# Optimization experiments

Hardware: AMD Instinct MI355X
Metric: run time of the kernel (lower is better)

Reference implementation:

```python
import jax, jax.numpy as jnp
import numpy as np

# SOLO decoupled-head postprocessing config (TrainConfig)
GRIDS = (40, 36, 24, 16, 12)
STRIDES = (4.0, 8.0, 16.0, 32.0, 64.0)
NMS_PRE = 500
SCORE_THR = 0.1
MASK_THR = 0.005
UPDATE_THR = 0.001
SIGMA = 2.0
MAX_PER_IMG = 100
NUM_CLASSES = 80


def _cell_meta():
    """Per-flattened-cell metadata across the 5 FPN levels (static)."""
    trans_diff, seg_diff, num_grids, strides = [], [], [], []
    t, s = 0, 0
    for g, st in zip(GRIDS, STRIDES):
        n = g * g
        trans_diff.append(np.full(n, t, np.int32))
        seg_diff.append(np.full(n, s, np.int32))
        num_grids.append(np.full(n, g, np.int32))
        strides.append(np.full(n, st, np.float32))
        t += n
        s += g
    return (jnp.asarray(np.concatenate(trans_diff)),
            jnp.asarray(np.concatenate(seg_diff)),
            jnp.asarray(np.concatenate(num_grids)),
            jnp.asarray(np.concatenate(strides)))


def setup_inputs() -> dict:
    key = jax.random.key(0)
    k1, k2, k3 = jax.random.split(key, 3)
    n_cells = sum(g * g for g in GRIDS)   # 3872
    n_rows = sum(GRIDS)                   # 128
    H, W = 200, 304                        # stride-4 map of an 800x1216 image
    return {
        "cate_preds": jax.random.uniform(k1, (n_cells, NUM_CLASSES), jnp.float32),
        "seg_preds_x": jax.random.uniform(k2, (n_rows, H, W), jnp.float32),
        "seg_preds_y": jax.random.uniform(k3, (n_rows, H, W), jnp.float32),
        "ori_h": 427,
        "ori_w": 640,
    }


def _matrix_nms(hardf, labels, scores, sum_masks):
    """Matrix NMS with gaussian decay. hardf: [n, h, w] float, descending scores."""
    n = hardf.shape[0]
    flat = hardf.reshape(n, -1)                      # [n, h*w]
    inter = flat @ flat.T                            # [n, n] pairwise intersection
    union = sum_masks[None, :] + sum_masks[:, None] - inter
    iou = jnp.where(union > 0, inter / jnp.maximum(union, 1e-12), 0.0)
    tri = jnp.triu(jnp.ones((n, n), jnp.float32), 1)  # cols > rows (strict upper)
    same = (labels[None, :] == labels[:, None]) & (labels[:, None] >= 0)
    decay_iou = iou * tri * same.astype(jnp.float32)  # [n, n]
    comp = decay_iou.max(axis=0)                      # max IoU with higher-scored same-class
    decay_m = jnp.exp(-SIGMA * decay_iou ** 2)
    comp_m = jnp.exp(-SIGMA * comp[:, None] ** 2)     # compensate[i, j] = f(comp[i])
    coeff = (decay_m / comp_m).min(axis=0)            # [n]
    return scores * coeff


def reference(cate_preds, seg_preds_x, seg_preds_y, ori_h, ori_w):
    trans_diff, seg_diff, num_grids, strides = _cell_meta()
    C = cate_preds.shape[1]
    flat = cate_preds.reshape(-1)
    flat = jnp.where(flat > SCORE_THR, flat, -1.0)
    scores, idx = jax.lax.top_k(flat, NMS_PRE)        # fixed-size candidate set
    loc = idx // C
    labels = (idx % C).astype(jnp.int32)
    valid = scores > SCORE_THR

    td, sd = trans_diff[loc], seg_diff[loc]
    ng, st = num_grids[loc], strides[loc]
    y_inds = (loc - td) // ng + sd
    x_inds = (loc - td) % ng + sd

    soft = seg_preds_x[x_inds] * seg_preds_y[y_inds]  # [N, H, W]
    hard = soft > MASK_THR
    sum_masks = hard.sum(axis=(1, 2)).astype(jnp.float32)
    keep = valid & (sum_masks > st)
    seg_score = (soft * hard).sum(axis=(1, 2)) / jnp.maximum(sum_masks, 1e-6)
    scores = jnp.where(keep, scores * seg_score, 0.0)
    keepf = keep.astype(jnp.float32)
    hardf = hard.astype(jnp.float32) * keepf[:, None, None]
    sum_masks = sum_masks * keepf
    labels = jnp.where(keep, labels, -1)

    # descending sort (matrix NMS assumes descending scores)
    order = jnp.argsort(-scores)
    scores, labels = scores[order], labels[order]
    soft, hardf, sum_masks = soft[order], hardf[order], sum_masks[order]

    scores = _matrix_nms(hardf, labels, scores, sum_masks)
    scores = jnp.where(scores > UPDATE_THR, scores, 0.0)

    top_scores, top_idx = jax.lax.top_k(scores, MAX_PER_IMG)
    top_soft = soft[top_idx]                          # [100, H, W]
    top_labels = labels[top_idx]

    H, W = top_soft.shape[1], top_soft.shape[2]
    up = jax.image.resize(top_soft, (MAX_PER_IMG, H * 4, W * 4), method="bilinear")
    up = jax.image.resize(up, (MAX_PER_IMG, ori_h, ori_w), method="bilinear")
    seg_masks = (up > MASK_THR).astype(jnp.float32)
    return seg_masks, top_labels, top_scores
```

## Files before the change

### kernel.cpp

```cpp
#include <hip/hip_runtime.h>
#include <stdint.h>

typedef unsigned int u32;
typedef unsigned long long u64;

#define NCELLS  3872
#define NCLS    80
#define NFLAT   309760
#define NPRE    500
#define NPAD    512
#define HH      200
#define WW      304
#define NPIX    60800
#define NWORDS  950
#define MSTRIDE 960
#define MAXOUT  100
#define OH      427
#define OW      640
#define MH      800
#define MW      1216
#define MAXG    4096
#define MAXPAIRS 16384
#define OUT_LBL 27328000
#define OUT_SCR 27328100
#define ROWS_PER_BLK 2
#define NRBLK 214

#define S_THR 0.1f
#define M_THR 0.005f
#define U_THR 0.001f

#define OFF_HIST1   0u
#define OFF_META    263168u
#define ZERO_BYTES  262144u
#define OFF_CAND    263424u
#define OFF_RAW     296192u
#define OFF_LOC     298240u
#define OFF_LABEL   300288u
#define OFF_XIND    302336u
#define OFF_YIND    304384u
#define OFF_STRIDE  306432u
#define OFF_SMF     308480u
#define OFF_SCORE   310528u
#define OFF_LABELK  312576u
#define OFF_ORDER   314624u
#define OFF_SSCORE  316672u
#define OFF_TOPC    318720u
#define OFF_PAIRI   319232u
#define OFF_PAIRIOU 384768u
#define OFF_W1YT0   450304u
#define OFF_W1YA    453504u
#define OFF_W1YB    456704u
#define OFF_W1XT0   459904u
#define OFF_W1XA    464768u
#define OFF_W1XB    469632u
#define OFF_W2YS    474496u
#define OFF_W2YW    476224u
#define OFF_W2XS    483072u
#define OFF_W2XW    485632u
#define OFF_MASKS   495872u
#define OFF_MASKT   4335872u
#define OFF_PARTD   8227072u
#define WS_NEED     12118272u

#define P_U32(off) ((u32*)(ws + (off)))
#define P_I32(off) ((int*)(ws + (off)))
#define P_F32(off) ((float*)(ws + (off)))
#define P_U64(off) ((u64*)(ws + (off)))

__device__ __forceinline__ void levelMeta(int loc, int& td, int& sd, int& ng, float& st) {
  if (loc < 1600)      { td = 0;    sd = 0;   ng = 40; st = 4.f;  }
  else if (loc < 2896) { td = 1600; sd = 40;  ng = 36; st = 8.f;  }
  else if (loc < 3472) { td = 2896; sd = 76;  ng = 24; st = 16.f; }
  else if (loc < 3728) { td = 3472; sd = 100; ng = 16; st = 32.f; }
  else                 { td = 3728; sd = 116; ng = 12; st = 64.f; }
}

__device__ __forceinline__ u32 vbin(float v) {
  int b = (int)(v * 65536.0f);
  if (b > 65535) b = 65535;
  if (b < 0) b = 0;
  return (u32)b;
}

__device__ __forceinline__ u64 shflx64(u64 v, int m) {
  u32 lo = (u32)v, hi = (u32)(v >> 32);
  lo = (u32)__shfl_xor((int)lo, m);
  hi = (u32)__shfl_xor((int)hi, m);
  return (((u64)hi) << 32) | lo;
}

__global__ void kh1(const float* __restrict__ cate, char* __restrict__ ws) {
  int i = blockIdx.x * 256 + threadIdx.x;
  if (i >= NFLAT / 4) return;
  float4 v = ((const float4*)cate)[i];
  u32* h = P_U32(OFF_HIST1);
  if (v.x > S_THR) atomicAdd(&h[vbin(v.x)], 1u);
  if (v.y > S_THR) atomicAdd(&h[vbin(v.y)], 1u);
  if (v.z > S_THR) atomicAdd(&h[vbin(v.z)], 1u);
  if (v.w > S_THR) atomicAdd(&h[vbin(v.w)], 1u);
}

__global__ __launch_bounds__(1024) void kselw(const float* __restrict__ cate, char* __restrict__ ws) {
  __shared__ u64 sk[MAXG];
  __shared__ u32 cs[1024];
  __shared__ u32 sfx[1024];
  __shared__ int cbS;
  __shared__ u32 aboveS;
  __shared__ u32 gcnt;
  __shared__ u32 cutS;
  int tid = threadIdx.x;
  const u32* h = P_U32(OFF_HIST1);
  u32 s = 0;
  for (int b = 0; b < 64; b++) s += h[tid * 64 + b];
  sfx[tid] = s;
  if (tid == 0) { cbS = -1; gcnt = 0; cutS = 0; }
  __syncthreads();
  for (int off = 1; off < 1024; off <<= 1) {
    u32 v = (tid + off < 1024) ? sfx[tid + off] : 0u;
    __syncthreads();
    sfx[tid] += v;
    __syncthreads();
  }
  u32 nxt = (tid < 1023) ? sfx[tid + 1] : 0u;
  if (sfx[tid] >= NPRE && nxt < NPRE) { cbS = tid; aboveS = nxt; }
  __syncthreads();
  if (cbS >= 0) {
    int cb = cbS;
    if (tid < 64) cs[tid] = h[cb * 64 + tid];
    __syncthreads();
    if (tid == 0) {
      u32 cum = aboveS;
      u32 bin = (u32)(cb * 64);
      for (int b = 63; b >= 0; b--) {
        u32 hb = cs[b];
        if (cum + hb >= NPRE) { bin = (u32)(cb * 64 + b); break; }
        cum += hb;
      }
      cutS = bin;
    }
  }
  __syncthreads();
  u32 cutbin = cutS;
  const float4* cate4 = (const float4*)cate;
  for (int i = tid; i < NFLAT / 4; i += 1024) {
    float4 v = cate4[i];
    #pragma unroll
    for (int q = 0; q < 4; q++) {
      float f = (q == 0) ? v.x : (q == 1) ? v.y : (q == 2) ? v.z : v.w;
      if (f > S_THR && vbin(f) >= cutbin) {
        u32 pos = atomicAdd(&gcnt, 1u);
        if (pos < MAXG) sk[pos] = (((u64)__float_as_uint(f)) << 32) | (u32)(~(u32)(i * 4 + q));
      }
    }
  }
  __syncthreads();
  int G = (int)gcnt; if (G > MAXG) G = MAXG;
  int n = NPAD;
  while (n < G) n <<= 1;
  for (int i = G + tid; i < n; i += 1024) sk[i] = 0ull;
  __syncthreads();
  if (n == NPAD) {
    u64 key = (tid < NPAD) ? sk[tid] : 0ull;
    __syncthreads();
    for (int k = 2; k <= NPAD; k <<= 1) {
      for (int j = k >> 1; j > 0; j >>= 1) {
        bool up = ((tid & k) == 0);
        u64 other;
        if (j < 64) {
          other = shflx64(key, j);
        } else {
          if (tid < NPAD) sk[tid] = key;
          __syncthreads();
          other = sk[(tid ^ j) & (NPAD - 1)];
          __syncthreads();
        }
        bool takeMax = (((tid & j) == 0) == up);
        u64 nk = takeMax ? (key > other ? key : other) : (key < other ? key : other);
        if (tid < NPAD) key = nk;
      }
    }
    if (tid < NPAD) sk[tid] = key;
    __syncthreads();
  } else {
    for (int k = 2; k <= n; k <<= 1) {
      for (int j = k >> 1; j > 0; j >>= 1) {
        for (int i = tid; i < n; i += 1024) {
          int l = i ^ j;
          if (l > i) {
            u64 a = sk[i], b = sk[l];
            bool sw = ((i & k) == 0) ? (a < b) : (a > b);
            if (sw) { sk[i] = b; sk[l] = a; }
          }
        }
        __syncthreads();
      }
    }
  }
  if (tid < NPAD) {
    float rawv = -1.f; int lab = -1, xi = 0, yi = 0; float st = 3.0e38f;
    if (tid < NPRE && tid < G) {
      u64 key = sk[tid];
      u32 b = (u32)(key >> 32);
      u32 idx = ~((u32)(key & 0xffffffffu));
      rawv = __uint_as_float(b);
      int loc = (int)(idx / (u32)NCLS);
      lab = (int)(idx - (u32)loc * NCLS);
      int td, sd, ng; levelMeta(loc, td, sd, ng, st);
      int rel = loc - td;
      int row = rel / ng;
      yi = row + sd;
      xi = (rel - row * ng) + sd;
    }
    P_F32(OFF_RAW)[tid] = rawv;
    P_I32(OFF_LABEL)[tid] = lab;
    P_I32(OFF_XIND)[tid] = xi;
    P_I32(OFF_YIND)[tid] = yi;
    P_F32(OFF_STRIDE)[tid] = st;
    P_F32(OFF_SCORE)[tid] = 0.f;
    P_I32(OFF_LABELK)[tid] = -1;
    P_F32(OFF_SMF)[tid] = 0.f;
  }
  int t = tid;
  for (int r = t; r < MH; r += 1024) {
    float s1 = ((float)r + 0.5f) * 0.25f - 0.5f;
    int t0 = (int)floorf(s1);
    float f = s1 - (float)t0;
    float wa = 1.f - f, wb = f;
    bool ia = (t0 >= 0) && (t0 < HH);
    bool ib = ((t0 + 1) >= 0) && ((t0 + 1) < HH);
    float tw = (ia ? wa : 0.f) + (ib ? wb : 0.f);
    float na = ia ? (wa / tw) : 0.f;
    float nb = ib ? (wb / tw) : 0.f;
    int base; float A, B;
    if (t0 < 0) { base = 0; A = nb; B = 0.f; }
    else if (t0 >= HH - 1) { base = HH - 2; A = 0.f; B = na; }
    else { base = t0; A = na; B = nb; }
    P_I32(OFF_W1YT0)[r] = base;
    P_F32(OFF_W1YA)[r] = A;
    P_F32(OFF_W1YB)[r] = B;
  }
  for (int c = t; c < MW; c += 1024) {
    float s1 = ((float)c + 0.5f) * 0.25f - 0.5f;
    int t0 = (int)floorf(s1);
    float f = s1 - (float)t0;
    float wa = 1.f - f, wb = f;
    bool ia = (t0 >= 0) && (t0 < WW);
    bool ib = ((t0 + 1) >= 0) && ((t0 + 1) < WW);
    float tw = (ia ? wa : 0.f) + (ib ? wb : 0.f);
    float na = ia ? (wa / tw) : 0.f;
    float nb = ib ? (wb / tw) : 0.f;
    int base; float A, B;
    if (t0 < 0) { base = 0; A = nb; B = 0.f; }
    else if (t0 >= WW - 1) { base = WW - 2; A = 0.f; B = na; }
    else { base = t0; A = na; B = nb; }
    P_I32(OFF_W1XT0)[c] = base;
    P_F32(OFF_W1XA)[c] = A;
    P_F32(OFF_W1XB)[c] = B;
  }
  for (int o = t; o < OH; o += 1024) {
    const float inv = (float)(800.0 / 427.0);
    float s2 = ((float)o + 0.5f) * inv - 0.5f;
    int rA = (int)ceilf(s2 - inv);
    int rB = (int)floorf(s2 + inv);
    if (rA < 0) rA = 0;
    if (rB > MH - 1) rB = MH - 1;
    float tot = 0.f;
    for (int r = rA; r <= rB; r++) {
      float x = fabsf(s2 - (float)r) / inv;
      float w = 1.f - x; if (w < 0.f) w = 0.f;
      tot += w;
    }
    int base = rA; if (base > MH - 4) base = MH - 4;
    float o4[4] = {0.f, 0.f, 0.f, 0.f};
    for (int r = rA; r <= rB; r++) {
      float x = fabsf(s2 - (float)r) / inv;
      float w = 1.f - x; if (w < 0.f) w = 0.f;
      o4[r - base] += w / tot;
    }
    P_I32(OFF_W2YS)[o] = base;
    float* wp = P_F32(OFF_W2YW) + o * 4;
    wp[0] = o4[0]; wp[1] = o4[1]; wp[2] = o4[2]; wp[3] = o4[3];
  }
  for (int o = t; o < OW; o += 1024) {
    const float inv = (float)(1216.0 / 640.0);
    float s2 = ((float)o + 0.5f) * inv - 0.5f;
    int rA = (int)ceilf(s2 - inv);
    int rB = (int)floorf(s2 + inv);
    if (rA < 0) rA = 0;
    if (rB > MW - 1) rB = MW - 1;
    float tot = 0.f;
    for (int r = rA; r <= rB; r++) {
      float x = fabsf(s2 - (float)r) / inv;
      float w = 1.f - x; if (w < 0.f) w = 0.f;
      tot += w;
    }
    int base = rA; if (base > MW - 4) base = MW - 4;
    float o4[4] = {0.f, 0.f, 0.f, 0.f};
    for (int r = rA; r <= rB; r++) {
      float x = fabsf(s2 - (float)r) / inv;
      float w = 1.f - x; if (w < 0.f) w = 0.f;
      o4[r - base] += w / tot;
    }
    P_I32(OFF_W2XS)[o] = base;
    float* wp = P_F32(OFF_W2XW) + o * 4;
    wp[0] = o4[0]; wp[1] = o4[1]; wp[2] = o4[2]; wp[3] = o4[3];
  }
}

__global__ __launch_bounds__(256) void kmaskA(const float* __restrict__ segx, const float* __restrict__ segy,
                                              char* __restrict__ ws) {
  __shared__ float lx[128 * 64];
  __shared__ float ly[128 * 64];
  int w0 = blockIdx.x;
  int base = w0 << 6;
  int tid = threadIdx.x;
  for (int idx = tid; idx < 128 * 64; idx += 256) {
    int r = idx >> 6, col = idx & 63;
    int sw = col ^ (r & 63);
    lx[(r << 6) + sw] = segx[(size_t)r * NPIX + base + col];
    ly[(r << 6) + sw] = segy[(size_t)r * NPIX + base + col];
  }
  __syncthreads();
  const int* xind = P_I32(OFF_XIND);
  const int* yind = P_I32(OFF_YIND);
  u64* maskT = P_U64(OFF_MASKT) + (size_t)w0 * NPAD;
  double* partD = (double*)(ws + OFF_PARTD) + (size_t)w0 * NPAD;
  for (int c = tid; c < NPRE; c += 256) {
    int xi = xind[c], yi = yind[c];
    const float* rx = &lx[xi << 6];
    const float* ry = &ly[yi << 6];
    int xk = xi & 63, yk = yi & 63;
    u32 lo = 0, hi = 0;
    double sum = 0.0;
    #pragma unroll 8
    for (int p = 0; p < 32; p++) {
      float s = rx[p ^ xk] * ry[p ^ yk];
      if (s > M_THR) { lo |= (1u << p); sum += (double)s; }
    }
    #pragma unroll 8
    for (int p = 32; p < 64; p++) {
      float s = rx[p ^ xk] * ry[p ^ yk];
      if (s > M_THR) { hi |= (1u << (p - 32)); sum += (double)s; }
    }
    maskT[c] = (((u64)hi) << 32) | lo;
    partD[c] = sum;
  }
}

__global__ __launch_bounds__(256) void kmaskBT(char* __restrict__ ws) {
  __shared__ u64 tile[64][65];
  int b = blockIdx.x;
  int tid = threadIdx.x;
  if (b < NPRE) {
    __shared__ double cd[256];
    __shared__ int ci[256];
    int c = b;
    const u64* maskT = P_U64(OFF_MASKT);
    const double* partD = (const double*)(ws + OFF_PARTD);
    double ds = 0.0; int cnt = 0;
    for (int w = tid; w < NWORDS; w += 256) {
      ds += partD[(size_t)w * NPAD + c];
      cnt += (int)__popcll(maskT[(size_t)w * NPAD + c]);
    }
    cd[tid] = ds; ci[tid] = cnt;
    __syncthreads();
    for (int s2 = 128; s2 > 0; s2 >>= 1) {
      if (tid < s2) { ci[tid] += ci[tid + s2]; cd[tid] += cd[tid + s2]; }
      __syncthreads();
    }
    if (tid == 0) {
      float sm = (float)ci[0];
      float rawv = P_F32(OFF_RAW)[c];
      bool valid = rawv > S_THR;
      bool keep = valid && (sm > P_F32(OFF_STRIDE)[c]);
      float ssf = (float)cd[0];
      float segsc = ssf / fmaxf(sm, 1e-6f);
      P_F32(OFF_SCORE)[c] = keep ? (rawv * segsc) : 0.f;
      P_F32(OFF_SMF)[c] = keep ? sm : 0.f;
      P_I32(OFF_LABELK)[c] = keep ? P_I32(OFF_LABEL)[c] : -1;
    }
  } else {
    int q = b - NPRE;
    int w0 = (q % 15) << 6;
    int c0 = (q / 15) << 6;
    const u64* maskT = P_U64(OFF_MASKT);
    for (int idx = tid; idx < 64 * 64; idx += 256) {
      int rw = idx >> 6, cc = idx & 63;
      int w = w0 + rw;
      tile[rw][cc] = (w < NWORDS) ? maskT[(size_t)w * NPAD + (c0 + cc)] : 0ull;
    }
    __syncthreads();
    u64* masks = P_U64(OFF_MASKS);
    for (int idx = tid; idx < 64 * 64; idx += 256) {
      int rc = idx >> 6, wwi = idx & 63;
      int c = c0 + rc, w = w0 + wwi;
      if (c < NPRE && w < NWORDS) masks[(size_t)c * MSTRIDE + w] = tile[wwi][rc];
    }
  }
}

__global__ __launch_bounds__(256) void kmask(const float* __restrict__ segx, const float* __restrict__ segy,
                                             char* __restrict__ ws) {
  int c = blockIdx.x;
  int tid = threadIdx.x;
  int lane = tid & 63, wv = tid >> 6;
  const float* X = segx + (size_t)P_I32(OFF_XIND)[c] * NPIX;
  const float* Y = segy + (size_t)P_I32(OFF_YIND)[c] * NPIX;
  u64* mrow = P_U64(OFF_MASKS) + (size_t)c * MSTRIDE;
  int cnt = 0;
  double ssum = 0.0;
  for (int w0 = wv; w0 < NWORDS; w0 += 4) {
    int p = (w0 << 6) + lane;
    float s = X[p] * Y[p];
    bool b = s > M_THR;
    u64 bal = __ballot(b ? 1 : 0);
    if (lane == 0) mrow[w0] = bal;
    if (b) { cnt++; ssum += (double)s; }
  }
  __shared__ int ci[256];
  __shared__ double cd[256];
  ci[tid] = cnt; cd[tid] = ssum;
  __syncthreads();
  for (int s2 = 128; s2 > 0; s2 >>= 1) {
    if (tid < s2) { ci[tid] += ci[tid + s2]; cd[tid] += cd[tid + s2]; }
    __syncthreads();
  }
  if (tid == 0) {
    float sm = (float)ci[0];
    float rawv = P_F32(OFF_RAW)[c];
    bool valid = rawv > S_THR;
    bool keep = valid && (sm > P_F32(OFF_STRIDE)[c]);
    float ssf = (float)cd[0];
    float segsc = ssf / fmaxf(sm, 1e-6f);
    P_F32(OFF_SCORE)[c] = keep ? (rawv * segsc) : 0.f;
    P_F32(OFF_SMF)[c] = keep ? sm : 0.f;
    P_I32(OFF_LABELK)[c] = keep ? P_I32(OFF_LABEL)[c] : -1;
  }
}

__global__ __launch_bounds__(512) void ksp(char* __restrict__ ws) {
  __shared__ u64 sk[NPAD];
  __shared__ short slab[NPAD];
  __shared__ u32 scan[NPAD];
  int t = threadIdx.x;
  float sc = (t < NPRE) ? P_F32(OFF_SCORE)[t] : 0.f;
  u64 key = (((u64)__float_as_uint(sc)) << 32) | (u32)(NPAD - 1 - t);
  for (int k = 2; k <= NPAD; k <<= 1) {
    for (int j = k >> 1; j > 0; j >>= 1) {
      bool up = ((t & k) == 0);
      u64 other;
      if (j < 64) {
        other = shflx64(key, j);
      } else {
        sk[t] = key;
        __syncthreads();
        other = sk[t ^ j];
        __syncthreads();
      }
      bool takeMax = (((t & j) == 0) == up);
      key = takeMax ? (key > other ? key : other) : (key < other ? key : other);
    }
  }
  int ord = NPAD - 1 - (int)(key & 0xffffffffu);
  P_I32(OFF_ORDER)[t] = ord;
  P_F32(OFF_SSCORE)[t] = __uint_as_float((u32)(key >> 32));
  const int* labelK = P_I32(OFF_LABELK);
  int lab = (t < NPRE) ? labelK[ord] : -1;
  slab[t] = (short)lab;
  __syncthreads();
  u32 cnt = 0;
  if (lab >= 0) {
    short lj = (short)lab;
    for (int i = 0; i < t; i++) if (slab[i] == lj) cnt++;
  }
  scan[t] = cnt;
  __syncthreads();
  for (int off = 1; off < NPAD; off <<= 1) {
    u32 v = (t >= off) ? scan[t - off] : 0u;
    __syncthreads();
    scan[t] += v;
    __syncthreads();
  }
  if (t == NPAD - 1) {
    u32 tot = scan[t];
    P_U32(OFF_META)[4] = (tot > MAXPAIRS) ? MAXPAIRS : tot;
  }
  if (lab >= 0 && cnt) {
    u32 pos = scan[t] - cnt;
    short lj = (short)lab;
    u32* pairI = P_U32(OFF_PAIRI);
    for (int i = 0; i < t; i++) {
      if (slab[i] == lj) {
        if (pos < MAXPAIRS) pairI[pos] = (((u32)i) << 16) | (u32)t;
        pos++;
      }
    }
  }
}

__global__ __launch_bounds__(64) void kpiou(char* __restrict__ ws) {
  int P = (int)P_U32(OFF_META)[4]; if (P > MAXPAIRS) P = MAXPAIRS;
  const int* order = P_I32(OFF_ORDER);
  const float* smf = P_F32(OFF_SMF);
  const u64* masks = P_U64(OFF_MASKS);
  for (int p = blockIdx.x; p < P; p += gridDim.x) {
    u32 ij = P_U32(OFF_PAIRI)[p];
    int oi = order[ij >> 16];
    int oj = order[ij & 0xffffu];
    const u64* mi = masks + (size_t)oi * MSTRIDE;
    const u64* mj = masks + (size_t)oj * MSTRIDE;
    int inter = 0;
    for (int w = threadIdx.x; w < NWORDS; w += 64)
      inter += (int)__popcll(mi[w] & mj[w]);
    for (int off = 32; off > 0; off >>= 1)
      inter += __shfl_down(inter, off);
    if (threadIdx.x == 0) {
      float fi = (float)inter;
      float uni = (smf[oj] + smf[oi]) - fi;
      float iou = (uni > 0.f) ? (fi / fmaxf(uni, 1e-12f)) : 0.f;
      P_F32(OFF_PAIRIOU)[p] = iou;
    }
  }
}

__global__ __launch_bounds__(512) void knms(char* __restrict__ ws, float* __restrict__ out) {
  __shared__ int compI[NPAD];
  __shared__ int coefI[NPAD];
  __shared__ u64 sk[NPAD];
  int t = threadIdx.x;
  int P = (int)P_U32(OFF_META)[4]; if (P > MAXPAIRS) P = MAXPAIRS;
  const u32* pairI = P_U32(OFF_PAIRI);
  const float* pairIou = P_F32(OFF_PAIRIOU);
  const float* sscore = P_F32(OFF_SSCORE);
  const int* order = P_I32(OFF_ORDER);
  const int* labelK = P_I32(OFF_LABELK);
  int* topc = P_I32(OFF_TOPC);
  compI[t] = 0;
  coefI[t] = __float_as_int(1.0f);
  __syncthreads();
  for (int p = t; p < P; p += 512) {
    int j = (int)(pairI[p] & 0xffffu);
    atomicMax(&compI[j], __float_as_int(pairIou[p]));
  }
  __syncthreads();
  for (int p = t; p < P; p += 512) {
    u32 ij = pairI[p];
    int i = (int)(ij >> 16), j = (int)(ij & 0xffffu);
    float x = pairIou[p];
    float c = __int_as_float(compI[i]);
    float x2 = x * x, c2 = c * c;
    float r = (float)exp(-2.0 * ((double)x2 - (double)c2));
    atomicMin(&coefI[j], __float_as_int(r));
  }
  __syncthreads();
  float ns = 0.f;
  if (t < NPRE) {
    ns = sscore[t] * __int_as_float(coefI[t]);
    ns = (ns > U_THR) ? ns : 0.f;
  }
  u64 key = (((u64)__float_as_uint(ns)) << 32) | (u32)(NPAD - 1 - t);
  for (int k = 2; k <= NPAD; k <<= 1) {
    for (int j = k >> 1; j > 0; j >>= 1) {
      bool up = ((t & k) == 0);
      u64 other;
      if (j < 64) {
        other = shflx64(key, j);
      } else {
        sk[t] = key;
        __syncthreads();
        other = sk[t ^ j];
        __syncthreads();
      }
      bool takeMax = (((t & j) == 0) == up);
      key = takeMax ? (key > other ? key : other) : (key < other ? key : other);
    }
  }
  if (t < MAXOUT) {
    int pos = NPAD - 1 - (int)(key & 0xffffffffu);
    int cand = order[pos];
    topc[t] = cand;
    out[OUT_LBL + t] = (float)labelK[cand];
    out[OUT_SCR + t] = __uint_as_float((u32)(key >> 32));
  }
}

__global__ __launch_bounds__(256) void kout(const float* __restrict__ segx, const float* __restrict__ segy,
                                            char* __restrict__ ws, float* __restrict__ out) {
  __shared__ float t1s[6][WW];
  __shared__ float yrs[2][MW];
  int flat = blockIdx.x;
  int w = (flat & 7) * 2675 + (flat >> 3);
  int kk = w / NRBLK;
  int r2 = w - kk * NRBLK;
  int oy0 = r2 * ROWS_PER_BLK;
  int nrow = (oy0 + 1 < OH) ? 2 : 1;
  int tid = threadIdx.x;
  int cand = P_I32(OFF_TOPC)[kk];
  const float* X = segx + (size_t)P_I32(OFF_XIND)[cand] * NPIX;
  const float* Y = segy + (size_t)P_I32(OFF_YIND)[cand] * NPIX;
  const int* w2ys = P_I32(OFF_W2YS);
  int rb = w2ys[oy0];
  const int* w1yT0 = P_I32(OFF_W1YT0);
  const float* w1yA = P_F32(OFF_W1YA);
  const float* w1yB = P_F32(OFF_W1YB);
  int smin = w1yT0[rb];
  float Ay[6], By[6]; int i0a[6];
  #pragma unroll
  for (int mr = 0; mr < 6; mr++) {
    int r = rb + mr; if (r > MH - 1) r = MH - 1;
    i0a[mr] = w1yT0[r] - smin;
    Ay[mr] = w1yA[r];
    By[mr] = w1yB[r];
  }
  {
    int r0 = smin;     if (r0 > HH - 1) r0 = HH - 1;
    int r1 = smin + 1; if (r1 > HH - 1) r1 = HH - 1;
    int r2s = smin + 2; if (r2s > HH - 1) r2s = HH - 1;
    int r3 = smin + 3; if (r3 > HH - 1) r3 = HH - 1;
    const float* X0 = X + r0 * WW; const float* Y0 = Y + r0 * WW;
    const float* X1 = X + r1 * WW; const float* Y1 = Y + r1 * WW;
    const float* X2 = X + r2s * WW; const float* Y2 = Y + r2s * WW;
    const float* X3 = X + r3 * WW; const float* Y3 = Y + r3 * WW;
    for (int u = tid; u < WW; u += 256) {
      float s0 = X0[u] * Y0[u];
      float s1 = X1[u] * Y1[u];
      float s2 = X2[u] * Y2[u];
      float s3 = X3[u] * Y3[u];
      #pragma unroll
      for (int mr = 0; mr < 6; mr++) {
        int i0 = i0a[mr];
        float sa, sb;
        if (i0 == 0)      { sa = s0; sb = s1; }
        else if (i0 == 1) { sa = s1; sb = s2; }
        else              { sa = s2; sb = s3; }
        t1s[mr][u] = fmaf(By[mr], sb, Ay[mr] * sa);
      }
    }
  }
  __syncthreads();
  const int* w1xT0 = P_I32(OFF_W1XT0);
  const float* w1xA = P_F32(OFF_W1XA);
  const float* w1xB = P_F32(OFF_W1XB);
  float4 wy0 = *(const float4*)(P_F32(OFF_W2YW) + oy0 * 4);
  int oy1 = (nrow == 2) ? (oy0 + 1) : oy0;
  float4 wy1 = *(const float4*)(P_F32(OFF_W2YW) + oy1 * 4);
  int off1 = w2ys[oy1] - rb;
  for (int cc = tid; cc < MW; cc += 256) {
    int u0 = w1xT0[cc];
    float xa = w1xA[cc], xb = w1xB[cc];
    float up0 = fmaf(xb, t1s[0][u0 + 1], xa * t1s[0][u0]);
    float up1 = fmaf(xb, t1s[1][u0 + 1], xa * t1s[1][u0]);
    float up2 = fmaf(xb, t1s[2][u0 + 1], xa * t1s[2][u0]);
    float up3 = fmaf(xb, t1s[3][u0 + 1], xa * t1s[3][u0]);
    float up4 = fmaf(xb, t1s[4][u0 + 1], xa * t1s[4][u0]);
    float up5 = fmaf(xb, t1s[5][u0 + 1], xa * t1s[5][u0]);
    float v0 = wy0.x * up0;
    v0 = fmaf(wy0.y, up1, v0);
    v0 = fmaf(wy0.z, up2, v0);
    v0 = fmaf(wy0.w, up3, v0);
    yrs[0][cc] = v0;
    if (nrow == 2) {
      float a, b2, c3, d;
      if (off1 == 1)      { a = up1; b2 = up2; c3 = up3; d = up4; }
      else if (off1 == 2) { a = up2; b2 = up3; c3 = up4; d = up5; }
      else                { a = up0; b2 = up1; c3 = up2; d = up3; }
      float v1 = wy1.x * a;
      v1 = fmaf(wy1.y, b2, v1);
      v1 = fmaf(wy1.z, c3, v1);
      v1 = fmaf(wy1.w, d, v1);
      yrs[1][cc] = v1;
    }
  }
  __syncthreads();
  const int* w2xS = P_I32(OFF_W2XS);
  size_t ob0 = ((size_t)kk * OH + oy0) * OW;
  size_t ob1 = ob0 + OW;
  for (int ox = tid; ox < OW; ox += 256) {
    int cb = w2xS[ox];
    float4 wx = *(const float4*)(P_F32(OFF_W2XW) + ox * 4);
    float a0 = wx.x * yrs[0][cb];
    a0 = fmaf(wx.y, yrs[0][cb + 1], a0);
    a0 = fmaf(wx.z, yrs[0][cb + 2], a0);
    a0 = fmaf(wx.w, yrs[0][cb + 3], a0);
    out[ob0 + ox] = (a0 > M_THR) ? 1.0f : 0.0f;
    if (nrow == 2) {
      float a1 = wx.x * yrs[1][cb];
      a1 = fmaf(wx.y, yrs[1][cb + 1], a1);
      a1 = fmaf(wx.z, yrs[1][cb + 2], a1);
      a1 = fmaf(wx.w, yrs[1][cb + 3], a1);
      out[ob1 + ox] = (a1 > M_THR) ? 1.0f : 0.0f;
    }
  }
}

extern "C" void kernel_launch(void* const* d_in, const int* in_sizes, int n_in,
                              void* d_out, int out_size, void* d_ws, size_t ws_size,
                              hipStream_t stream) {
  (void)in_sizes; (void)n_in; (void)out_size;
  const float* cate = (const float*)d_in[0];
  const float* segx = (const float*)d_in[1];
  const float* segy = (const float*)d_in[2];
  char* ws = (char*)d_ws;
  float* out = (float*)d_out;
  const bool bigws = (ws_size >= (size_t)WS_NEED);

  hipMemsetAsync(ws, 0, ZERO_BYTES, stream);

  dim3 gFlat4((NFLAT / 4 + 255) / 256);
  hipLaunchKernelGGL(kh1, gFlat4, dim3(256), 0, stream, cate, ws);
  hipLaunchKernelGGL(kselw, dim3(1), dim3(1024), 0, stream, cate, ws);
  if (bigws) {
    hipLaunchKernelGGL(kmaskA, dim3(NWORDS), dim3(256), 0, stream, segx, segy, ws);
    hipLaunchKernelGGL(kmaskBT, dim3(NPRE + 120), dim3(256), 0, stream, ws);
  } else {
    hipLaunchKernelGGL(kmask, dim3(NPRE), dim3(256), 0, stream, segx, segy, ws);
  }
  hipLaunchKernelGGL(ksp, dim3(1), dim3(512), 0, stream, ws);
  hipLaunchKernelGGL(kpiou, dim3(2048), dim3(64), 0, stream, ws);
  hipLaunchKernelGGL(knms, dim3(1), dim3(512), 0, stream, ws, out);
  hipLaunchKernelGGL(kout, dim3(MAXOUT * NRBLK), dim3(256), 0, stream, segx, segy, ws, out);
}
```

Measured before the change: 264.3 us.

## Merge selection and NMS stages into cooperative kernels with grid syncs

Replaces the separate histogram and single-block top-k selection kernels with one cooperative kernel that builds the histogram grid-wide, finds the cut bin in block 0, and compacts candidates in parallel across the grid. It also fuses mask transposition, score sorting and pair building, pairwise IoU and matrix NMS into a second cooperative kernel separated by grid.sync. The aim is to cut kernel launch gaps and the serial candidate scan that used to run in one block. In exchange it adds grid-wide barriers and needs every block of a 620-block, 512-thread cooperative grid to be resident at once, and the launch fails if they are not.

```diff
diff --git a/kernel.cpp b/kernel.cpp
--- a/kernel.cpp
+++ b/kernel.cpp
@@ -1,5 +1,8 @@
 #include <hip/hip_runtime.h>
+#include <hip/hip_cooperative_groups.h>
 #include <stdint.h>
+
+namespace cg = cooperative_groups;
 
 typedef unsigned int u32;
 typedef unsigned long long u64;
@@ -32,10 +35,9 @@
 
 #define OFF_HIST1   0u
 #define OFF_META    263168u
-#define ZERO_BYTES  262144u
+#define ZERO_BYTES  263232u
 #define OFF_CAND    263424u
 #define OFF_RAW     296192u
-#define OFF_LOC     298240u
 #define OFF_LABEL   300288u
 #define OFF_XIND    302336u
 #define OFF_YIND    304384u
@@ -90,117 +92,31 @@
   return (((u64)hi) << 32) | lo;
 }
 
-__global__ void kh1(const float* __restrict__ cate, char* __restrict__ ws) {
-  int i = blockIdx.x * 256 + threadIdx.x;
-  if (i >= NFLAT / 4) return;
-  float4 v = ((const float4*)cate)[i];
-  u32* h = P_U32(OFF_HIST1);
-  if (v.x > S_THR) atomicAdd(&h[vbin(v.x)], 1u);
-  if (v.y > S_THR) atomicAdd(&h[vbin(v.y)], 1u);
-  if (v.z > S_THR) atomicAdd(&h[vbin(v.z)], 1u);
-  if (v.w > S_THR) atomicAdd(&h[vbin(v.w)], 1u);
-}
-
-__global__ __launch_bounds__(1024) void kselw(const float* __restrict__ cate, char* __restrict__ ws) {
-  __shared__ u64 sk[MAXG];
-  __shared__ u32 cs[1024];
-  __shared__ u32 sfx[1024];
-  __shared__ int cbS;
-  __shared__ u32 aboveS;
-  __shared__ u32 gcnt;
-  __shared__ u32 cutS;
-  int tid = threadIdx.x;
-  const u32* h = P_U32(OFF_HIST1);
-  u32 s = 0;
-  for (int b = 0; b < 64; b++) s += h[tid * 64 + b];
-  sfx[tid] = s;
-  if (tid == 0) { cbS = -1; gcnt = 0; cutS = 0; }
-  __syncthreads();
-  for (int off = 1; off < 1024; off <<= 1) {
-    u32 v = (tid + off < 1024) ? sfx[tid + off] : 0u;
-    __syncthreads();
-    sfx[tid] += v;
-    __syncthreads();
-  }
-  u32 nxt = (tid < 1023) ? sfx[tid + 1] : 0u;
-  if (sfx[tid] >= NPRE && nxt < NPRE) { cbS = tid; aboveS = nxt; }
-  __syncthreads();
-  if (cbS >= 0) {
-    int cb = cbS;
-    if (tid < 64) cs[tid] = h[cb * 64 + tid];
-    __syncthreads();
-    if (tid == 0) {
-      u32 cum = aboveS;
-      u32 bin = (u32)(cb * 64);
-      for (int b = 63; b >= 0; b--) {
-        u32 hb = cs[b];
-        if (cum + hb >= NPRE) { bin = (u32)(cb * 64 + b); break; }
-        cum += hb;
-      }
-      cutS = bin;
-    }
-  }
-  __syncthreads();
-  u32 cutbin = cutS;
-  const float4* cate4 = (const float4*)cate;
-  for (int i = tid; i < NFLAT / 4; i += 1024) {
-    float4 v = cate4[i];
-    #pragma unroll
-    for (int q = 0; q < 4; q++) {
-      float f = (q == 0) ? v.x : (q == 1) ? v.y : (q == 2) ? v.z : v.w;
-      if (f > S_THR && vbin(f) >= cutbin) {
-        u32 pos = atomicAdd(&gcnt, 1u);
-        if (pos < MAXG) sk[pos] = (((u64)__float_as_uint(f)) << 32) | (u32)(~(u32)(i * 4 + q));
-      }
-    }
-  }
-  __syncthreads();
-  int G = (int)gcnt; if (G > MAXG) G = MAXG;
-  int n = NPAD;
-  while (n < G) n <<= 1;
-  for (int i = G + tid; i < n; i += 1024) sk[i] = 0ull;
-  __syncthreads();
-  if (n == NPAD) {
-    u64 key = (tid < NPAD) ? sk[tid] : 0ull;
-    __syncthreads();
-    for (int k = 2; k <= NPAD; k <<= 1) {
-      for (int j = k >> 1; j > 0; j >>= 1) {
-        bool up = ((tid & k) == 0);
-        u64 other;
-        if (j < 64) {
-          other = shflx64(key, j);
-        } else {
-          if (tid < NPAD) sk[tid] = key;
-          __syncthreads();
-          other = sk[(tid ^ j) & (NPAD - 1)];
-          __syncthreads();
-        }
-        bool takeMax = (((tid & j) == 0) == up);
-        u64 nk = takeMax ? (key > other ? key : other) : (key < other ? key : other);
-        if (tid < NPAD) key = nk;
-      }
-    }
-    if (tid < NPAD) sk[tid] = key;
-    __syncthreads();
-  } else {
-    for (int k = 2; k <= n; k <<= 1) {
-      for (int j = k >> 1; j > 0; j >>= 1) {
-        for (int i = tid; i < n; i += 1024) {
-          int l = i ^ j;
-          if (l > i) {
-            u64 a = sk[i], b = sk[l];
-            bool sw = ((i & k) == 0) ? (a < b) : (a > b);
-            if (sw) { sk[i] = b; sk[l] = a; }
-          }
-        }
+__device__ __forceinline__ u64 bitonic512(u64 key, int tid, u64* sk) {
+  for (int k = 2; k <= NPAD; k <<= 1) {
+    for (int j = k >> 1; j > 0; j >>= 1) {
+      bool up = ((tid & k) == 0);
+      u64 other;
+      if (j < 64) {
+        other = shflx64(key, j);
+      } else {
+        sk[tid] = key;
+        __syncthreads();
+        other = sk[tid ^ j];
         __syncthreads();
       }
-    }
-  }
-  if (tid < NPAD) {
+      bool takeMax = (((tid & j) == 0) == up);
+      key = takeMax ? (key > other ? key : other) : (key < other ? key : other);
+    }
+  }
+  return key;
+}
+
+__device__ void selwTail(char* ws, const u64* skSorted, int G, int tid) {
+  {
     float rawv = -1.f; int lab = -1, xi = 0, yi = 0; float st = 3.0e38f;
     if (tid < NPRE && tid < G) {
-      u64 key = sk[tid];
+      u64 key = skSorted[tid];
       u32 b = (u32)(key >> 32);
       u32 idx = ~((u32)(key & 0xffffffffu));
       rawv = __uint_as_float(b);
@@ -222,7 +138,7 @@
     P_F32(OFF_SMF)[tid] = 0.f;
   }
   int t = tid;
-  for (int r = t; r < MH; r += 1024) {
+  for (int r = t; r < MH; r += 512) {
     float s1 = ((float)r + 0.5f) * 0.25f - 0.5f;
     int t0 = (int)floorf(s1);
     float f = s1 - (float)t0;
@@ -240,7 +156,7 @@
     P_F32(OFF_W1YA)[r] = A;
     P_F32(OFF_W1YB)[r] = B;
   }
-  for (int c = t; c < MW; c += 1024) {
+  for (int c = t; c < MW; c += 512) {
     float s1 = ((float)c + 0.5f) * 0.25f - 0.5f;
     int t0 = (int)floorf(s1);
     float f = s1 - (float)t0;
@@ -258,7 +174,7 @@
     P_F32(OFF_W1XA)[c] = A;
     P_F32(OFF_W1XB)[c] = B;
   }
-  for (int o = t; o < OH; o += 1024) {
+  for (int o = t; o < OH; o += 512) {
     const float inv = (float)(800.0 / 427.0);
     float s2 = ((float)o + 0.5f) * inv - 0.5f;
     int rA = (int)ceilf(s2 - inv);
@@ -282,7 +198,7 @@
     float* wp = P_F32(OFF_W2YW) + o * 4;
     wp[0] = o4[0]; wp[1] = o4[1]; wp[2] = o4[2]; wp[3] = o4[3];
   }
-  for (int o = t; o < OW; o += 1024) {
+  for (int o = t; o < OW; o += 512) {
     const float inv = (float)(1216.0 / 640.0);
     float s2 = ((float)o + 0.5f) * inv - 0.5f;
     int rA = (int)ceilf(s2 - inv);
@@ -305,6 +221,106 @@
     P_I32(OFF_W2XS)[o] = base;
     float* wp = P_F32(OFF_W2XW) + o * 4;
     wp[0] = o4[0]; wp[1] = o4[1]; wp[2] = o4[2]; wp[3] = o4[3];
+  }
+}
+
+__global__ __launch_bounds__(512) void kcoopA(const float* __restrict__ cate, char* __restrict__ ws) {
+  cg::grid_group grid = cg::this_grid();
+  __shared__ u64 sk[MAXG];
+  __shared__ u32 cs[512];
+  __shared__ u32 sfx[512];
+  __shared__ int cbS;
+  __shared__ u32 aboveS;
+  int tid = threadIdx.x;
+  int gtid = blockIdx.x * 512 + tid;
+  int gstride = gridDim.x * 512;
+  u32* h = P_U32(OFF_HIST1);
+  const float4* cate4 = (const float4*)cate;
+  for (int i = gtid; i < NFLAT / 4; i += gstride) {
+    float4 v = cate4[i];
+    if (v.x > S_THR) atomicAdd(&h[vbin(v.x)], 1u);
+    if (v.y > S_THR) atomicAdd(&h[vbin(v.y)], 1u);
+    if (v.z > S_THR) atomicAdd(&h[vbin(v.z)], 1u);
+    if (v.w > S_THR) atomicAdd(&h[vbin(v.w)], 1u);
+  }
+  grid.sync();
+  if (blockIdx.x == 0) {
+    u32 s = 0;
+    for (int b = 0; b < 128; b++) s += h[tid * 128 + b];
+    sfx[tid] = s;
+    if (tid == 0) cbS = -1;
+    __syncthreads();
+    for (int off = 1; off < 512; off <<= 1) {
+      u32 v = (tid + off < 512) ? sfx[tid + off] : 0u;
+      __syncthreads();
+      sfx[tid] += v;
+      __syncthreads();
+    }
+    u32 nxt = (tid < 511) ? sfx[tid + 1] : 0u;
+    if (sfx[tid] >= NPRE && nxt < NPRE) { cbS = tid; aboveS = nxt; }
+    __syncthreads();
+    u32* meta = P_U32(OFF_META);
+    if (cbS < 0) {
+      if (tid == 0) meta[2] = 0u;
+    } else {
+      int cb = cbS;
+      if (tid < 128) cs[tid] = h[cb * 128 + tid];
+      __syncthreads();
+      if (tid == 0) {
+        u32 cum = aboveS;
+        u32 bin = (u32)(cb * 128);
+        for (int b = 127; b >= 0; b--) {
+          u32 hb = cs[b];
+          if (cum + hb >= NPRE) { bin = (u32)(cb * 128 + b); break; }
+          cum += hb;
+        }
+        meta[2] = bin;
+      }
+    }
+  }
+  grid.sync();
+  u32 key = P_U32(OFF_META)[2];
+  u64* cand = P_U64(OFF_CAND);
+  u32* cntp = &P_U32(OFF_META)[3];
+  for (int i = gtid; i < NFLAT / 4; i += gstride) {
+    float4 v = cate4[i];
+    #pragma unroll
+    for (int q = 0; q < 4; q++) {
+      float f = (q == 0) ? v.x : (q == 1) ? v.y : (q == 2) ? v.z : v.w;
+      if (f > S_THR && vbin(f) >= key) {
+        u32 pos = atomicAdd(cntp, 1u);
+        if (pos < MAXG) cand[pos] = (((u64)__float_as_uint(f)) << 32) | (u32)(~(u32)(i * 4 + q));
+      }
+    }
+  }
+  grid.sync();
+  if (blockIdx.x == 0) {
+    int G = (int)P_U32(OFF_META)[3]; if (G > MAXG) G = MAXG;
+    int n = NPAD;
+    while (n < G) n <<= 1;
+    if (n == NPAD) {
+      u64 k0 = (tid < G) ? cand[tid] : 0ull;
+      k0 = bitonic512(k0, tid, sk);
+      sk[tid] = k0;
+      __syncthreads();
+    } else {
+      for (int i = tid; i < n; i += 512) sk[i] = (i < G) ? cand[i] : 0ull;
+      __syncthreads();
+      for (int k = 2; k <= n; k <<= 1) {
+        for (int j = k >> 1; j > 0; j >>= 1) {
+          for (int i = tid; i < n; i += 512) {
+            int l = i ^ j;
+            if (l > i) {
+              u64 a = sk[i], b = sk[l];
+              bool sw = ((i & k) == 0) ? (a < b) : (a > b);
+              if (sw) { sk[i] = b; sk[l] = a; }
+            }
+          }
+          __syncthreads();
+        }
+      }
+    }
+    selwTail(ws, sk, G, tid);
   }
 }
 
@@ -348,24 +364,30 @@
   }
 }
 
-__global__ __launch_bounds__(256) void kmaskBT(char* __restrict__ ws) {
+__global__ __launch_bounds__(512) void kcoopB(char* __restrict__ ws, float* __restrict__ out) {
+  cg::grid_group grid = cg::this_grid();
   __shared__ u64 tile[64][65];
-  int b = blockIdx.x;
+  __shared__ double cd[512];
+  __shared__ int ci[512];
+  __shared__ u64 sk[NPAD];
+  __shared__ short slab[NPAD];
+  __shared__ u32 scan[NPAD];
+  __shared__ int compI[NPAD];
+  __shared__ int coefI[NPAD];
   int tid = threadIdx.x;
-  if (b < NPRE) {
-    __shared__ double cd[256];
-    __shared__ int ci[256];
-    int c = b;
-    const u64* maskT = P_U64(OFF_MASKT);
+  int bid = blockIdx.x;
+  const u64* maskT = P_U64(OFF_MASKT);
+  if (bid < NPRE) {
+    int c = bid;
     const double* partD = (const double*)(ws + OFF_PARTD);
     double ds = 0.0; int cnt = 0;
-    for (int w = tid; w < NWORDS; w += 256) {
+    for (int w = tid; w < NWORDS; w += 512) {
       ds += partD[(size_t)w * NPAD + c];
       cnt += (int)__popcll(maskT[(size_t)w * NPAD + c]);
     }
     cd[tid] = ds; ci[tid] = cnt;
     __syncthreads();
-    for (int s2 = 128; s2 > 0; s2 >>= 1) {
+    for (int s2 = 256; s2 > 0; s2 >>= 1) {
       if (tid < s2) { ci[tid] += ci[tid + s2]; cd[tid] += cd[tid + s2]; }
       __syncthreads();
     }
@@ -381,21 +403,131 @@
       P_I32(OFF_LABELK)[c] = keep ? P_I32(OFF_LABEL)[c] : -1;
     }
   } else {
-    int q = b - NPRE;
+    int q = bid - NPRE;
     int w0 = (q % 15) << 6;
     int c0 = (q / 15) << 6;
-    const u64* maskT = P_U64(OFF_MASKT);
-    for (int idx = tid; idx < 64 * 64; idx += 256) {
+    for (int idx = tid; idx < 64 * 64; idx += 512) {
       int rw = idx >> 6, cc = idx & 63;
       int w = w0 + rw;
       tile[rw][cc] = (w < NWORDS) ? maskT[(size_t)w * NPAD + (c0 + cc)] : 0ull;
     }
     __syncthreads();
     u64* masks = P_U64(OFF_MASKS);
-    for (int idx = tid; idx < 64 * 64; idx += 256) {
+    for (int idx = tid; idx < 64 * 64; idx += 512) {
       int rc = idx >> 6, wwi = idx & 63;
       int c = c0 + rc, w = w0 + wwi;
       if (c < NPRE && w < NWORDS) masks[(size_t)c * MSTRIDE + w] = tile[wwi][rc];
+    }
+  }
+  grid.sync();
+  if (bid == 0) {
+    float sc = (tid < NPRE) ? P_F32(OFF_SCORE)[tid] : 0.f;
+    u64 key = (((u64)__float_as_uint(sc)) << 32) | (u32)(NPAD - 1 - tid);
+    key = bitonic512(key, tid, sk);
+    int ord = NPAD - 1 - (int)(key & 0xffffffffu);
+    P_I32(OFF_ORDER)[tid] = ord;
+    P_F32(OFF_SSCORE)[tid] = __uint_as_float((u32)(key >> 32));
+    const int* labelK = P_I32(OFF_LABELK);
+    int lab = (tid < NPRE) ? labelK[ord] : -1;
+    slab[tid] = (short)lab;
+    __syncthreads();
+    u32 cnt = 0;
+    if (lab >= 0) {
+      short lj = (short)lab;
+      for (int i = 0; i < tid; i++) if (slab[i] == lj) cnt++;
+    }
+    scan[tid] = cnt;
+    __syncthreads();
+    for (int off = 1; off < NPAD; off <<= 1) {
+      u32 v = (tid >= off) ? scan[tid - off] : 0u;
+      __syncthreads();
+      scan[tid] += v;
+      __syncthreads();
+    }
+    if (tid == NPAD - 1) {
+      u32 tot = scan[tid];
+      P_U32(OFF_META)[4] = (tot > MAXPAIRS) ? MAXPAIRS : tot;
+    }
+    if (lab >= 0 && cnt) {
+      u32 pos = scan[tid] - cnt;
+      short lj = (short)lab;
+      u32* pairI = P_U32(OFF_PAIRI);
+      for (int i = 0; i < tid; i++) {
+        if (slab[i] == lj) {
+          if (pos < MAXPAIRS) pairI[pos] = (((u32)i) << 16) | (u32)tid;
+          pos++;
+        }
+      }
+    }
+  }
+  grid.sync();
+  {
+    int P = (int)P_U32(OFF_META)[4]; if (P > MAXPAIRS) P = MAXPAIRS;
+    const int* order = P_I32(OFF_ORDER);
+    const float* smf = P_F32(OFF_SMF);
+    const u64* masks = P_U64(OFF_MASKS);
+    int wid = tid >> 6, lane = tid & 63;
+    int gw = bid * 8 + wid;
+    int gwstride = gridDim.x * 8;
+    for (int p = gw; p < P; p += gwstride) {
+      u32 ij = P_U32(OFF_PAIRI)[p];
+      int oi = order[ij >> 16];
+      int oj = order[ij & 0xffffu];
+      const u64* mi = masks + (size_t)oi * MSTRIDE;
+      const u64* mj = masks + (size_t)oj * MSTRIDE;
+      int inter = 0;
+      for (int w = lane; w < NWORDS; w += 64)
+        inter += (int)__popcll(mi[w] & mj[w]);
+      for (int off = 32; off > 0; off >>= 1)
+        inter += __shfl_down(inter, off);
+      if (lane == 0) {
+        float fi = (float)inter;
+        float uni = (smf[oj] + smf[oi]) - fi;
+        float iou = (uni > 0.f) ? (fi / fmaxf(uni, 1e-12f)) : 0.f;
+        P_F32(OFF_PAIRIOU)[p] = iou;
+      }
+    }
+  }
+  grid.sync();
+  if (bid == 0) {
+    int P = (int)P_U32(OFF_META)[4]; if (P > MAXPAIRS) P = MAXPAIRS;
+    const u32* pairI = P_U32(OFF_PAIRI);
+    const float* pairIou = P_F32(OFF_PAIRIOU);
+    const float* sscore = P_F32(OFF_SSCORE);
+    const int* order = P_I32(OFF_ORDER);
+    const int* labelK = P_I32(OFF_LABELK);
+    int* topc = P_I32(OFF_TOPC);
+    compI[tid] = 0;
+    coefI[tid] = __float_as_int(1.0f);
+    __syncthreads();
+    for (int p = tid; p < P; p += 512) {
+      int j = (int)(pairI[p] & 0xffffu);
+      atomicMax(&compI[j], __float_as_int(pairIou[p]));
+    }
+    __syncthreads();
+    for (int p = tid; p < P; p += 512) {
+      u32 ij = pairI[p];
+      int i = (int)(ij >> 16), j = (int)(ij & 0xffffu);
+      float x = pairIou[p];
+      float c = __int_as_float(compI[i]);
+      float x2 = x * x, c2 = c * c;
+      float r = (float)exp(-2.0 * ((double)x2 - (double)c2));
+      atomicMin(&coefI[j], __float_as_int(r));
+    }
+    __syncthreads();
+    float ns = 0.f;
+    if (tid < NPRE) {
+      ns = sscore[tid] * __int_as_float(coefI[tid]);
+      ns = (ns > U_THR) ? ns : 0.f;
+    }
+    u64 key = (((u64)__float_as_uint(ns)) << 32) | (u32)(NPAD - 1 - tid);
+    key = bitonic512(key, tid, sk);
+    if (tid < MAXOUT) {
+      int pos = NPAD - 1 - (int)(key & 0xffffffffu);
+      int cand = order[pos];
+      topc[tid] = cand;
+      out[OUT_LBL + tid] = (float)labelK[cand];
+      out[OUT_SCR + tid] = __uint_as_float((u32)(key >> 32));
     }
   }
 }
@@ -446,22 +578,7 @@
   int t = threadIdx.x;
   float sc = (t < NPRE) ? P_F32(OFF_SCORE)[t] : 0.f;
   u64 key = (((u64)__float_as_uint(sc)) << 32) | (u32)(NPAD - 1 - t);
-  for (int k = 2; k <= NPAD; k <<= 1) {
-    for (int j = k >> 1; j > 0; j >>= 1) {
-      bool up = ((t & k) == 0);
-      u64 other;
-      if (j < 64) {
-        other = shflx64(key, j);
-      } else {
-        sk[t] = key;
-        __syncthreads();
-        other = sk[t ^ j];
-        __syncthreads();
-      }
-      bool takeMax = (((t & j) == 0) == up);
-      key = takeMax ? (key > other ? key : other) : (key < other ? key : other);
-    }
-  }
+  key = bitonic512(key, t, sk);
   int ord = NPAD - 1 - (int)(key & 0xffffffffu);
   P_I32(OFF_ORDER)[t] = ord;
   P_F32(OFF_SSCORE)[t] = __uint_as_float((u32)(key >> 32));
@@ -560,22 +677,7 @@
     ns = (ns > U_THR) ? ns : 0.f;
   }
   u64 key = (((u64)__float_as_uint(ns)) << 32) | (u32)(NPAD - 1 - t);
-  for (int k = 2; k <= NPAD; k <<= 1) {
-    for (int j = k >> 1; j > 0; j >>= 1) {
-      bool up = ((t & k) == 0);
-      u64 other;
-      if (j < 64) {
-        other = shflx64(key, j);
-      } else {
-        sk[t] = key;
-        __syncthreads();
-        other = sk[t ^ j];
-        __syncthreads();
-      }
-      bool takeMax = (((t & j) == 0) == up);
-      key = takeMax ? (key > other ? key : other) : (key < other ? key : other);
-    }
-  }
+  key = bitonic512(key, t, sk);
   if (t < MAXOUT) {
     int pos = NPAD - 1 - (int)(key & 0xffffffffu);
     int cand = order[pos];
@@ -707,17 +809,19 @@
 
   hipMemsetAsync(ws, 0, ZERO_BYTES, stream);
 
-  dim3 gFlat4((NFLAT / 4 + 255) / 256);
-  hipLaunchKernelGGL(kh1, gFlat4, dim3(256), 0, stream, cate, ws);
-  hipLaunchKernelGGL(kselw, dim3(1), dim3(1024), 0, stream, cate, ws);
+  {
+    void* argsA[] = { (void*)&cate, (void*)&ws };
+    hipLaunchCooperativeKernel((void*)kcoopA, dim3(152), dim3(512), argsA, 0, stream);
+  }
   if (bigws) {
     hipLaunchKernelGGL(kmaskA, dim3(NWORDS), dim3(256), 0, stream, segx, segy, ws);
-    hipLaunchKernelGGL(kmaskBT, dim3(NPRE + 120), dim3(256), 0, stream, ws);
+    void* argsB[] = { (void*)&ws, (void*)&out };
+    hipLaunchCooperativeKernel((void*)kcoopB, dim3(NPRE + 120), dim3(512), argsB, 0, stream);
   } else {
     hipLaunchKernelGGL(kmask, dim3(NPRE), dim3(256), 0, stream, segx, segy, ws);
-  }
-  hipLaunchKernelGGL(ksp, dim3(1), dim3(512), 0, stream, ws);
-  hipLaunchKernelGGL(kpiou, dim3(2048), dim3(64), 0, stream, ws);
-  hipLaunchKernelGGL(knms, dim3(1), dim3(512), 0, stream, ws, out);
+    hipLaunchKernelGGL(ksp, dim3(1), dim3(512), 0, stream, ws);
+    hipLaunchKernelGGL(kpiou, dim3(2048), dim3(64), 0, stream, ws);
+    hipLaunchKernelGGL(knms, dim3(1), dim3(512), 0, stream, ws, out);
+  }
   hipLaunchKernelGGL(kout, dim3(MAXOUT * NRBLK), dim3(256), 0, stream, segx, segy, ws, out);
 }
```

Result: slower. 478.2 us (+80.9%).
